# Kernel tuning notes

Hardware: AMD Instinct MI355X
Metric: run time of the kernel (lower is better)

## Reference

```python
import jax, jax.numpy as jnp
import numpy as np

# Topologies derived from init kwargs (inputs=64, outputs=64, state=512, net1 hidden=[512])
D = 64 + 64 + 512                      # 640 = concat(input, prev_output, state)
NET1 = [D, 512, 64]
NET3 = [D] + NET1 + [512]              # [640, 640, 512, 64, 512] (code reuses mutated net1 topo)
W_TOTAL = sum(NET3[j] * NET3[j + 1] for j in range(len(NET3) - 1))  # 802816
B_TOTAL = sum(NET3[1:])                # 1728
NET2 = [D] + NET1 + [W_TOTAL + B_TOTAL]  # [640, 640, 512, 64, 804544]


def _leaky(v):
    return jnp.where(v >= 0, v, 0.01 * v)


def setup_inputs() -> dict:
    key = jax.random.key(0)
    ks = jax.random.split(key, 16)
    inp = {
        "x": jax.random.normal(ks[0], (64,), jnp.float32),
        "prev_output": jnp.zeros((64,), jnp.float32),
        "state": jnp.zeros((512,), jnp.float32),
    }
    # net1 params (Linear stores W as [out, in])
    for i in range(len(NET1) - 1):
        inp[f"net1_w{i}"] = jax.random.normal(ks[1 + i], (NET1[i + 1], NET1[i]), jnp.float32) * 0.02
        inp[f"net1_b{i}"] = jnp.zeros((NET1[i + 1],), jnp.float32)
    # net2 params
    for i in range(len(NET2) - 1):
        inp[f"net2_w{i}"] = jax.random.normal(ks[5 + i], (NET2[i + 1], NET2[i]), jnp.float32) * 0.02
        inp[f"net2_b{i}"] = jnp.zeros((NET2[i + 1],), jnp.float32)
    return inp


def reference(x, prev_output, state,
              net1_w0, net1_b0, net1_w1, net1_b1,
              net2_w0, net2_b0, net2_w1, net2_b1,
              net2_w2, net2_b2, net2_w3, net2_b3):
    inpt = jnp.concatenate([x, prev_output, state])  # [640]

    # net2: hypernetwork producing flattened weights+biases for net3
    h = _leaky(net2_w0 @ inpt + net2_b0)
    h = _leaky(net2_w1 @ h + net2_b1)
    h = _leaky(net2_w2 @ h + net2_b2)
    x2 = jnp.tanh(net2_w3 @ h + net2_b3) * 0.5       # [W_TOTAL + B_TOTAL]
    weights = x2[:W_TOTAL]
    bias = x2[W_TOTAL:]

    # net3: apply generated weights sequentially (state update)
    x3 = inpt
    wi, bi = 0, 0
    for j in range(1, len(NET3)):
        out_d, in_d = NET3[j], NET3[j - 1]
        W = weights[wi:wi + out_d * in_d].reshape(out_d, in_d)
        b = bias[bi:bi + out_d]
        x3 = W @ x3 + b                               # 1D: x3 @ W.T == W @ x3
        if j != len(NET3) - 1:
            x3 = _leaky(x3)
        wi += out_d * in_d
        bi += out_d
    new_state = x3                                    # [512]

    # net1: output head
    h1 = _leaky(net1_w0 @ inpt + net1_b0)
    out = net1_w1 @ h1 + net1_b1                      # [64]

    # torch forward returns only `out`; new_state is the persistent buffer
    # update. We concatenate both so the full step math is observable.
    return jnp.concatenate([out, new_state])          # [576]
```

## Files before the change

kernel.cpp:

```cpp
#include <hip/hip_runtime.h>
#include <math.h>


#define WS_H0    0
#define WS_H1N1  640
#define WS_H1N2  1152
#define WS_H2    1664
#define WS_INPT  1728
#define WS_X3A   2368
#define WS_X3B   3008
#define WS_X3C   3520
#define WS_T     4096

#define N_ROWS   804544
#define N_WAVES  12571

__device__ __forceinline__ float leaky_f(float v) { return v >= 0.0f ? v : 0.01f * v; }

__device__ __forceinline__ float inpt_at(int i, const float* x, const float* po, const float* st) {
  return i < 64 ? x[i] : (i < 128 ? po[i - 64] : st[i - 128]);
}

__device__ __forceinline__ float half_tanh(float d) {
  float t = exp2f(d * 2.8853900817779268f);
  return 0.5f - __builtin_amdgcn_rcpf(t + 1.0f);
}

template <int IN>
__device__ __forceinline__ float row_dot(const float* __restrict__ wrow, const float* s_in, int lane) {
  const float4* w4 = (const float4*)wrow;
  const float4* s4 = (const float4*)s_in;
  float acc = 0.f;
  for (int j = lane; j < IN / 4; j += 64) {
    float4 a = w4[j];
    float4 b = s4[j];
    acc += a.x * b.x + a.y * b.y + a.z * b.z + a.w * b.w;
  }
  for (int off = 32; off; off >>= 1) acc += __shfl_xor(acc, off, 64);
  return acc;
}

__global__ __launch_bounds__(256) void k1a(const float* __restrict__ x, const float* __restrict__ po,
                                           const float* __restrict__ st,
                                           const float* __restrict__ w2_0, const float* __restrict__ b2_0,
                                           const float* __restrict__ w1_0, const float* __restrict__ b1_0,
                                           float* __restrict__ ws) {
  __shared__ __align__(16) float s_in[640];
  for (int i = threadIdx.x; i < 640; i += 256) {
    float v = inpt_at(i, x, po, st);
    s_in[i] = v;
    ws[WS_INPT + i] = v;
  }
  __syncthreads();
  int wave = threadIdx.x >> 6, lane = threadIdx.x & 63;
  int o = blockIdx.x * 4 + wave;
  const float* wrow;
  float bias;
  float* dst;
  if (o < 640) {
    wrow = w2_0 + (long long)o * 640; bias = b2_0[o]; dst = ws + WS_H0 + o;
  } else {
    int oo = o - 640;
    wrow = w1_0 + (long long)oo * 640; bias = b1_0[oo]; dst = ws + WS_H1N1 + oo;
  }
  float acc = row_dot<640>(wrow, s_in, lane);
  if (lane == 0) *dst = leaky_f(acc + bias);
}

__global__ __launch_bounds__(256) void k1b(const float* __restrict__ w2_1, const float* __restrict__ b2_1,
                                           const float* __restrict__ w1_1, const float* __restrict__ b1_1,
                                           float* __restrict__ ws, float* __restrict__ out) {
  __shared__ __align__(16) float s_h0[640];
  __shared__ __align__(16) float s_h1[512];
  for (int i = threadIdx.x; i < 640; i += 256) s_h0[i] = ws[WS_H0 + i];
  for (int i = threadIdx.x; i < 512; i += 256) s_h1[i] = ws[WS_H1N1 + i];
  __syncthreads();
  int wave = threadIdx.x >> 6, lane = threadIdx.x & 63;
  int o = blockIdx.x * 4 + wave;
  if (o < 512) {
    float acc = row_dot<640>(w2_1 + (long long)o * 640, s_h0, lane);
    if (lane == 0) ws[WS_H1N2 + o] = leaky_f(acc + b2_1[o]);
  } else {
    int oo = o - 512;
    float acc = row_dot<512>(w1_1 + (long long)oo * 512, s_h1, lane);
    if (lane == 0) out[oo] = acc + b1_1[oo];
  }
}

__global__ __launch_bounds__(256) void k1c(const float* __restrict__ w2_2, const float* __restrict__ b2_2,
                                           float* __restrict__ ws) {
  __shared__ __align__(16) float s_h[512];
  for (int i = threadIdx.x; i < 512; i += 256) s_h[i] = ws[WS_H1N2 + i];
  __syncthreads();
  int wave = threadIdx.x >> 6, lane = threadIdx.x & 63;
  int o = blockIdx.x * 4 + wave;
  float acc = row_dot<512>(w2_2 + (long long)o * 512, s_h, lane);
  if (lane == 0) ws[WS_H2 + o] = leaky_f(acc + b2_2[o]);
}

__global__ __launch_bounds__(256) void bigT(const float* __restrict__ w3, const float* __restrict__ b3,
                                            const float* __restrict__ h2p, float* __restrict__ t) {
  int wid = blockIdx.x * 4 + (threadIdx.x >> 6);
  if (wid >= N_WAVES) return;
  const int lane = threadIdx.x & 63;
  const int g = lane >> 4;
  const int gl = lane & 15;
  float4 hv = ((const float4*)h2p)[gl];
  const long long base = (long long)wid * 64;
  const float4* wp = (const float4*)(w3 + (base << 6));
  float4 v[16];
#pragma unroll
  for (int q = 0; q < 16; q++) v[q] = wp[((q * 4 + g) << 4) + gl];
#pragma unroll
  for (int q = 0; q < 16; q++) {
    float d = v[q].x * hv.x + v[q].y * hv.y + v[q].z * hv.z + v[q].w * hv.w;
    d += __shfl_xor(d, 1, 64);
    d += __shfl_xor(d, 2, 64);
    d += __shfl_xor(d, 4, 64);
    d += __shfl_xor(d, 8, 64);
    if (gl == 0) {
      long long r = base + q * 4 + g;
      t[r] = half_tanh(d + b3[r]);
    }
  }
}

template <int IN, bool LEAKY>
__global__ __launch_bounds__(256) void gml(const float* __restrict__ t, const float* __restrict__ x3in,
                                           float* __restrict__ x3out, long long wi, long long brow,
                                           int OUT) {
  __shared__ __align__(16) float s_in[IN];
  for (int i = threadIdx.x; i < IN; i += 256) s_in[i] = x3in[i];
  __syncthreads();
  int wave = threadIdx.x >> 6, lane = threadIdx.x & 63;
  int o = blockIdx.x * 4 + wave;
  if (o >= OUT) return;
  float acc = row_dot<IN>(t + wi + (long long)o * IN, s_in, lane);
  if (lane == 0) {
    acc += t[brow + o];
    x3out[o] = LEAKY ? leaky_f(acc) : acc;
  }
}

extern "C" void kernel_launch(void* const* d_in, const int* in_sizes, int n_in,
                              void* d_out, int out_size, void* d_ws, size_t ws_size,
                              hipStream_t stream) {
  const float* x    = (const float*)d_in[0];
  const float* po   = (const float*)d_in[1];
  const float* st   = (const float*)d_in[2];
  const float* w1_0 = (const float*)d_in[3];
  const float* b1_0 = (const float*)d_in[4];
  const float* w1_1 = (const float*)d_in[5];
  const float* b1_1 = (const float*)d_in[6];
  const float* w2_0 = (const float*)d_in[7];
  const float* b2_0 = (const float*)d_in[8];
  const float* w2_1 = (const float*)d_in[9];
  const float* b2_1 = (const float*)d_in[10];
  const float* w2_2 = (const float*)d_in[11];
  const float* b2_2 = (const float*)d_in[12];
  const float* w3   = (const float*)d_in[13];
  const float* b3   = (const float*)d_in[14];
  float* ws  = (float*)d_ws;
  float* out = (float*)d_out;
  float* t   = ws + WS_T;

  k1a<<<288, 256, 0, stream>>>(x, po, st, w2_0, b2_0, w1_0, b1_0, ws);
  k1b<<<144, 256, 0, stream>>>(w2_1, b2_1, w1_1, b1_1, ws, out);
  k1c<<<16, 256, 0, stream>>>(w2_2, b2_2, ws);
  bigT<<<(N_WAVES + 3) / 4, 256, 0, stream>>>(w3, b3, ws + WS_H2, t);
  gml<640, true><<<160, 256, 0, stream>>>(t, ws + WS_INPT, ws + WS_X3A, 0LL, 802816LL, 640);
  gml<640, true><<<128, 256, 0, stream>>>(t, ws + WS_X3A, ws + WS_X3B, 409600LL, 803456LL, 512);
  gml<512, true><<<16, 256, 0, stream>>>(t, ws + WS_X3B, ws + WS_X3C, 737280LL, 803968LL, 64);
  gml<64, false><<<128, 256, 0, stream>>>(t, ws + WS_X3C, out + 64, 770048LL, 804032LL, 512);
}
```

Baseline: 340.0 us.

## Fuse MLP trunk and net3 layers with grid barriers, fold layer-1 into bigT

Merges the three net1/net2 trunk kernels into one cooperative kernel that uses atomic-counter grid barriers, and the last three generated-weight layers into a second one. It also folds the first generated layer (640x640) into the big weight-generation kernel: generated weights are multiplied by the input on the fly and accumulated with atomics, so that slice is never written to memory and read back. The aim is to cut launch overhead and about 1.6 MB of workspace traffic. In exchange it relies on all blocks being co-resident for the spin barriers, and float atomic accumulation order is non-deterministic.

```diff
diff --git a/kernel.cpp b/kernel.cpp
--- a/kernel.cpp
+++ b/kernel.cpp
@@ -6,14 +6,16 @@
 #define WS_H1N1  640
 #define WS_H1N2  1152
 #define WS_H2    1664
-#define WS_INPT  1728
 #define WS_X3A   2368
-#define WS_X3B   3008
-#define WS_X3C   3520
+#define WS_CNT   3008
+#define WS_X3B   3072
+#define WS_X3C   3584
 #define WS_T     4096
 
 #define N_ROWS   804544
 #define N_WAVES  12571
+#define L1_ROWS  409600
+#define L1_WAVES 6400
 
 __device__ __forceinline__ float leaky_f(float v) { return v >= 0.0f ? v : 0.01f * v; }
 
@@ -24,6 +26,19 @@
 __device__ __forceinline__ float half_tanh(float d) {
   float t = exp2f(d * 2.8853900817779268f);
   return 0.5f - __builtin_amdgcn_rcpf(t + 1.0f);
+}
+
+__device__ __forceinline__ void gbar(unsigned* cnt, unsigned target) {
+  __syncthreads();
+  if (threadIdx.x == 0) {
+    __threadfence();
+    atomicAdd(cnt, 1u);
+    while (__hip_atomic_load(cnt, __ATOMIC_RELAXED, __HIP_MEMORY_SCOPE_AGENT) < target) {
+      __builtin_amdgcn_s_sleep(2);
+    }
+    __threadfence();
+  }
+  __syncthreads();
 }
 
 template <int IN>
@@ -40,77 +55,88 @@
   return acc;
 }
 
-__global__ __launch_bounds__(256) void k1a(const float* __restrict__ x, const float* __restrict__ po,
-                                           const float* __restrict__ st,
-                                           const float* __restrict__ w2_0, const float* __restrict__ b2_0,
-                                           const float* __restrict__ w1_0, const float* __restrict__ b1_0,
-                                           float* __restrict__ ws) {
+__global__ __launch_bounds__(256) void trunkCoop(
+    const float* __restrict__ x, const float* __restrict__ po, const float* __restrict__ st,
+    const float* __restrict__ w2_0, const float* __restrict__ b2_0,
+    const float* __restrict__ w2_1, const float* __restrict__ b2_1,
+    const float* __restrict__ w2_2, const float* __restrict__ b2_2,
+    const float* __restrict__ w1_0, const float* __restrict__ b1_0,
+    const float* __restrict__ w1_1, const float* __restrict__ b1_1,
+    float* __restrict__ ws, float* __restrict__ out, unsigned* __restrict__ cnt) {
   __shared__ __align__(16) float s_in[640];
-  for (int i = threadIdx.x; i < 640; i += 256) {
-    float v = inpt_at(i, x, po, st);
-    s_in[i] = v;
-    ws[WS_INPT + i] = v;
-  }
-  __syncthreads();
-  int wave = threadIdx.x >> 6, lane = threadIdx.x & 63;
-  int o = blockIdx.x * 4 + wave;
-  const float* wrow;
-  float bias;
-  float* dst;
-  if (o < 640) {
-    wrow = w2_0 + (long long)o * 640; bias = b2_0[o]; dst = ws + WS_H0 + o;
-  } else {
-    int oo = o - 640;
-    wrow = w1_0 + (long long)oo * 640; bias = b1_0[oo]; dst = ws + WS_H1N1 + oo;
-  }
-  float acc = row_dot<640>(wrow, s_in, lane);
-  if (lane == 0) *dst = leaky_f(acc + bias);
-}
-
-__global__ __launch_bounds__(256) void k1b(const float* __restrict__ w2_1, const float* __restrict__ b2_1,
-                                           const float* __restrict__ w1_1, const float* __restrict__ b1_1,
-                                           float* __restrict__ ws, float* __restrict__ out) {
   __shared__ __align__(16) float s_h0[640];
   __shared__ __align__(16) float s_h1[512];
-  for (int i = threadIdx.x; i < 640; i += 256) s_h0[i] = ws[WS_H0 + i];
-  for (int i = threadIdx.x; i < 512; i += 256) s_h1[i] = ws[WS_H1N1 + i];
-  __syncthreads();
-  int wave = threadIdx.x >> 6, lane = threadIdx.x & 63;
-  int o = blockIdx.x * 4 + wave;
-  if (o < 512) {
-    float acc = row_dot<640>(w2_1 + (long long)o * 640, s_h0, lane);
-    if (lane == 0) ws[WS_H1N2 + o] = leaky_f(acc + b2_1[o]);
-  } else {
-    int oo = o - 512;
-    float acc = row_dot<512>(w1_1 + (long long)oo * 512, s_h1, lane);
-    if (lane == 0) out[oo] = acc + b1_1[oo];
-  }
-}
-
-__global__ __launch_bounds__(256) void k1c(const float* __restrict__ w2_2, const float* __restrict__ b2_2,
-                                           float* __restrict__ ws) {
-  __shared__ __align__(16) float s_h[512];
-  for (int i = threadIdx.x; i < 512; i += 256) s_h[i] = ws[WS_H1N2 + i];
-  __syncthreads();
-  int wave = threadIdx.x >> 6, lane = threadIdx.x & 63;
-  int o = blockIdx.x * 4 + wave;
-  float acc = row_dot<512>(w2_2 + (long long)o * 512, s_h, lane);
-  if (lane == 0) ws[WS_H2 + o] = leaky_f(acc + b2_2[o]);
+  __shared__ __align__(16) float s_h2[512];
+  const int tid = threadIdx.x;
+  const int wave = tid >> 6, lane = tid & 63;
+  const int gw = blockIdx.x * 4 + wave;
+
+  for (int i = tid; i < 640; i += 256) s_in[i] = inpt_at(i, x, po, st);
+  __syncthreads();
+#pragma unroll
+  for (int r = 0; r < 3; r++) {
+    int o = gw + r * 512;
+    if (o < 640) {
+      float acc = row_dot<640>(w2_0 + (long long)o * 640, s_in, lane);
+      if (lane == 0) ws[WS_H0 + o] = leaky_f(acc + b2_0[o]);
+    } else if (o < 1152) {
+      int oo = o - 640;
+      float acc = row_dot<640>(w1_0 + (long long)oo * 640, s_in, lane);
+      if (lane == 0) ws[WS_H1N1 + oo] = leaky_f(acc + b1_0[oo]);
+    }
+  }
+  gbar(cnt + 0, 128);
+
+  for (int i = tid; i < 640; i += 256) s_h0[i] = ws[WS_H0 + i];
+  for (int i = tid; i < 512; i += 256) s_h1[i] = ws[WS_H1N1 + i];
+  __syncthreads();
+  {
+    int o = gw;
+    if (o < 512) {
+      float acc = row_dot<640>(w2_1 + (long long)o * 640, s_h0, lane);
+      if (lane == 0) ws[WS_H1N2 + o] = leaky_f(acc + b2_1[o]);
+    }
+    if (gw < 64) {
+      float acc = row_dot<512>(w1_1 + (long long)gw * 512, s_h1, lane);
+      if (lane == 0) out[gw] = acc + b1_1[gw];
+    }
+  }
+  gbar(cnt + 1, 128);
+
+  for (int i = tid; i < 512; i += 256) s_h2[i] = ws[WS_H1N2 + i];
+  __syncthreads();
+  if (gw < 64) {
+    float acc = row_dot<512>(w2_2 + (long long)gw * 512, s_h2, lane);
+    if (lane == 0) ws[WS_H2 + gw] = leaky_f(acc + b2_2[gw]);
+  }
 }
 
 __global__ __launch_bounds__(256) void bigT(const float* __restrict__ w3, const float* __restrict__ b3,
-                                            const float* __restrict__ h2p, float* __restrict__ t) {
-  int wid = blockIdx.x * 4 + (threadIdx.x >> 6);
+                                            const float* __restrict__ x, const float* __restrict__ po,
+                                            const float* __restrict__ st,
+                                            float* __restrict__ ws, float* __restrict__ t) {
+  __shared__ __align__(16) float s_inpt[640];
+  for (int i = threadIdx.x; i < 640; i += 256) s_inpt[i] = inpt_at(i, x, po, st);
+  __syncthreads();
+
+  const int wid = blockIdx.x * 4 + (threadIdx.x >> 6);
   if (wid >= N_WAVES) return;
   const int lane = threadIdx.x & 63;
   const int g = lane >> 4;
   const int gl = lane & 15;
-  float4 hv = ((const float4*)h2p)[gl];
+  const float4 hv = ((const float4*)(ws + WS_H2))[gl];
   const long long base = (long long)wid * 64;
   const float4* wp = (const float4*)(w3 + (base << 6));
+
+  const bool isL1 = (wid < L1_WAVES);
+  const int o_l1 = wid / 10;
+  const int ibase = (wid % 10) * 64;
+
   float4 v[16];
 #pragma unroll
   for (int q = 0; q < 16; q++) v[q] = wp[((q * 4 + g) << 4) + gl];
+
+  float acc = 0.0f;
 #pragma unroll
   for (int q = 0; q < 16; q++) {
     float d = v[q].x * hv.x + v[q].y * hv.y + v[q].z * hv.z + v[q].w * hv.w;
@@ -120,25 +146,65 @@
     d += __shfl_xor(d, 8, 64);
     if (gl == 0) {
       long long r = base + q * 4 + g;
-      t[r] = half_tanh(d + b3[r]);
-    }
-  }
-}
-
-template <int IN, bool LEAKY>
-__global__ __launch_bounds__(256) void gml(const float* __restrict__ t, const float* __restrict__ x3in,
-                                           float* __restrict__ x3out, long long wi, long long brow,
-                                           int OUT) {
-  __shared__ __align__(16) float s_in[IN];
-  for (int i = threadIdx.x; i < IN; i += 256) s_in[i] = x3in[i];
-  __syncthreads();
-  int wave = threadIdx.x >> 6, lane = threadIdx.x & 63;
-  int o = blockIdx.x * 4 + wave;
-  if (o >= OUT) return;
-  float acc = row_dot<IN>(t + wi + (long long)o * IN, s_in, lane);
-  if (lane == 0) {
-    acc += t[brow + o];
-    x3out[o] = LEAKY ? leaky_f(acc) : acc;
+      float tv = half_tanh(d + b3[r]);
+      if (isL1) acc += tv * s_inpt[ibase + q * 4 + g];
+      else t[r] = tv;
+    }
+  }
+  if (isL1) {
+    acc += __shfl_xor(acc, 16, 64);
+    acc += __shfl_xor(acc, 32, 64);
+    if (lane == 0) atomicAdd(&ws[WS_X3A + o_l1], acc);
+  }
+}
+
+__global__ __launch_bounds__(256) void gmlCoop(const float* __restrict__ t, float* __restrict__ ws,
+                                               float* __restrict__ out, unsigned* __restrict__ cnt) {
+  __shared__ __align__(16) float s_a[640];
+  __shared__ __align__(16) float s_b[512];
+  __shared__ float s_red[4];
+  const int tid = threadIdx.x;
+  const int wave = tid >> 6, lane = tid & 63;
+  const int gw = blockIdx.x * 4 + wave;
+
+  for (int i = tid; i < 640; i += 256) s_a[i] = leaky_f(ws[WS_X3A + i] + t[802816 + i]);
+  __syncthreads();
+#pragma unroll
+  for (int r = 0; r < 2; r++) {
+    int o = gw + r * 256;
+    float acc = row_dot<640>(t + 409600 + (long long)o * 640, s_a, lane);
+    if (lane == 0) ws[WS_X3B + o] = leaky_f(acc + t[803456 + o]);
+  }
+  gbar(cnt + 2, 64);
+
+  for (int i = tid; i < 512; i += 256) s_b[i] = ws[WS_X3B + i];
+  __syncthreads();
+  {
+    const int o = blockIdx.x;
+    const float4* row = (const float4*)(t + 737280 + (long long)o * 512);
+    const float4* bb = (const float4*)s_b;
+    float a = 0.f;
+    for (int j = tid; j < 128; j += 256) {
+      float4 wv = row[j], bv = bb[j];
+      a += wv.x * bv.x + wv.y * bv.y + wv.z * bv.z + wv.w * bv.w;
+    }
+    for (int off = 32; off; off >>= 1) a += __shfl_xor(a, off, 64);
+    if (lane == 0) s_red[wave] = a;
+    __syncthreads();
+    if (tid == 0) {
+      float tot = s_red[0] + s_red[1] + s_red[2] + s_red[3];
+      ws[WS_X3C + o] = leaky_f(tot + t[803968 + o]);
+    }
+  }
+  gbar(cnt + 3, 64);
+
+  float xc = ws[WS_X3C + lane];
+#pragma unroll
+  for (int r = 0; r < 2; r++) {
+    int o = gw + r * 256;
+    float a = t[770048 + (long long)o * 64 + lane] * xc;
+    for (int off = 32; off; off >>= 1) a += __shfl_xor(a, off, 64);
+    if (lane == 0) out[64 + o] = a + t[804032 + o];
   }
 }
 
@@ -163,13 +229,12 @@
   float* ws  = (float*)d_ws;
   float* out = (float*)d_out;
   float* t   = ws + WS_T;
-
-  k1a<<<288, 256, 0, stream>>>(x, po, st, w2_0, b2_0, w1_0, b1_0, ws);
-  k1b<<<144, 256, 0, stream>>>(w2_1, b2_1, w1_1, b1_1, ws, out);
-  k1c<<<16, 256, 0, stream>>>(w2_2, b2_2, ws);
-  bigT<<<(N_WAVES + 3) / 4, 256, 0, stream>>>(w3, b3, ws + WS_H2, t);
-  gml<640, true><<<160, 256, 0, stream>>>(t, ws + WS_INPT, ws + WS_X3A, 0LL, 802816LL, 640);
-  gml<640, true><<<128, 256, 0, stream>>>(t, ws + WS_X3A, ws + WS_X3B, 409600LL, 803456LL, 512);
-  gml<512, true><<<16, 256, 0, stream>>>(t, ws + WS_X3B, ws + WS_X3C, 737280LL, 803968LL, 64);
-  gml<64, false><<<128, 256, 0, stream>>>(t, ws + WS_X3C, out + 64, 770048LL, 804032LL, 512);
-}
+  unsigned* cnt = (unsigned*)(ws + WS_CNT);
+
+  hipMemsetAsync(ws + WS_X3A, 0, (640 + 16) * sizeof(float), stream);
+
+  trunkCoop<<<128, 256, 0, stream>>>(x, po, st, w2_0, b2_0, w2_1, b2_1, w2_2, b2_2,
+                                     w1_0, b1_0, w1_1, b1_1, ws, out, cnt);
+  bigT<<<(N_WAVES + 3) / 4, 256, 0, stream>>>(w3, b3, x, po, st, ws, t);
+  gmlCoop<<<64, 256, 0, stream>>>(t, ws, out, cnt);
+}
```

After: 368.8 us. 8.5% more time.
